# Performance work log

Hardware: AMD Instinct MI355X
Metric: run time of the kernel (lower is better)

Reference implementation:

```python
import jax, jax.numpy as jnp
import numpy as np

B, L, D = 2, 2048, 1024
K, M = 32, 4
H = D // K
AH = 4            # anchor heads
DH = K - AH       # decay heads
CK = 4            # conv kernel size
TOTAL = 2 * D + K + K * M


def setup_inputs() -> dict:
    key = jax.random.key(0)
    ks = jax.random.split(key, 7)
    x = jax.random.normal(ks[0], (B, L, D), jnp.float32)
    mask = jnp.ones((B, L), jnp.float32)
    W_in = jax.random.normal(ks[1], (D, TOTAL), jnp.float32) * 0.02
    conv_w = jax.random.normal(ks[2], (CK, TOTAL), jnp.float32) * 0.1  # depthwise taps
    conv_b = jnp.zeros((TOTAL,), jnp.float32)
    grid = np.linspace(-np.pi / 3, np.pi / 3, M).astype(np.float32)
    theta_base = jnp.asarray(np.tile(grid.reshape(1, 1, 1, 1, M), (1, 1, K, 1, 1)))
    theta_resid_scale = jnp.full((K,), 0.1, jnp.float32)
    dr = np.geomspace(0.001, 0.1, DH).astype(np.float32)
    decay_slopes = jnp.asarray(np.log(np.exp(dr) - 1.0).astype(np.float32))
    ar = np.geomspace(0.01, 0.1, AH).astype(np.float32)
    anchor_slopes = jnp.asarray(np.log(np.exp(ar) - 1.0).astype(np.float32))
    score_scale = jnp.ones((K,), jnp.float32)
    norm_scale = jnp.ones((2 * H * M,), jnp.float32)
    gl = float((2.0 / (H * M + H)) ** 0.5)  # glorot std
    W_re = jax.random.normal(ks[3], (H * M, H), jnp.float32) * gl
    W_im = jax.random.normal(ks[4], (H * M, H), jnp.float32) * gl
    W_out = jax.random.normal(ks[5], (D, D), jnp.float32) * 0.02
    return dict(x=x, mask=mask, W_in=W_in, conv_w=conv_w, conv_b=conv_b,
                theta_base=theta_base, theta_resid_scale=theta_resid_scale,
                decay_slopes=decay_slopes, anchor_slopes=anchor_slopes,
                score_scale=score_scale, norm_scale=norm_scale,
                W_re=W_re, W_im=W_im, W_out=W_out)


def _forward(x, mask, W_in, conv_w, conv_b, theta_base, theta_resid_scale,
             decay_slopes, anchor_slopes, score_scale, norm_scale, W_re, W_im, W_out):
    b, l, d = x.shape
    z = x @ W_in  # (b,l,TOTAL)
    # causal depthwise conv, kernel size CK
    zp = jnp.pad(z, ((0, 0), (CK - 1, 0), (0, 0)))
    z = sum(zp[:, t:t + l, :] * conv_w[t] for t in range(CK)) + conv_b

    x_val = z[..., :D].reshape(b, l, K, H)
    x_gate = jax.nn.silu(z[..., D:2 * D])
    s_raw = z[..., 2 * D:2 * D + K].reshape(b, l, K, 1)
    theta_raw = z[..., 2 * D + K:].reshape(b, l, K, M)

    theta_delta = theta_raw / (1.0 + jnp.abs(theta_raw))
    theta_dyn = theta_base + theta_resid_scale.reshape(1, 1, K, 1, 1) * (
        theta_delta.reshape(b, l, K, 1, M) * jnp.float32(np.pi / 3))

    m = mask[:, :, None, None]
    s_raw = s_raw * m
    x_val = x_val * m

    pos = jnp.arange(l, dtype=jnp.float32)
    slopes_d = jax.nn.softplus(decay_slopes).reshape(1, 1, DH, 1)
    dist_d = jnp.maximum(jnp.float32(l - 1) - pos, 0.0)[None, :, None, None]
    w_decay = jnp.exp(-slopes_d * dist_d)
    slopes_a = jax.nn.softplus(anchor_slopes).reshape(1, 1, AH, 1)
    w_anchor = jnp.exp(-slopes_a * pos[None, :, None, None])
    time_weight = jnp.concatenate([w_decay, w_anchor], axis=2)  # (1,l,K,1)

    p = jnp.exp(jnp.clip(score_scale[None, None, :, None] * s_raw, -20.0, 20.0))
    p = p * m

    phi = x_val[..., None] * theta_dyn  # (b,l,K,H,M)
    cos_b = jnp.cos(phi)
    sin_b = jnp.sin(phi)
    p_w = (p * time_weight)[..., None]  # (b,l,K,1,1)

    flat = (b, l, K * H * M)
    merged = jnp.concatenate([
        (p_w * cos_b).reshape(flat),
        (p_w * sin_b).reshape(flat),
        jnp.broadcast_to(p_w, (b, l, K, H, M)).reshape(flat)], axis=-1)
    cs = jnp.cumsum(merged, axis=1)
    num_re, num_im, den = jnp.split(cs, 3, axis=-1)
    inv_den = 1.0 / jnp.maximum(den, jnp.float32(1e-4))
    re = (num_re * inv_den).reshape(b, l, K, H * M)
    im = (num_im * inv_den).reshape(b, l, K, H * M)

    mean_sq = (jnp.sum(re * re, axis=-1) + jnp.sum(im * im, axis=-1)) * (1.0 / (2.0 * H * M))
    rsq = jax.lax.rsqrt(mean_sq[..., None] + 1e-5)
    y = (re * rsq * norm_scale[:H * M]) @ W_re + (im * rsq * norm_scale[H * M:]) @ W_im  # (b,l,K,H)
    y = y.reshape(b, l, D)
    return (y * x_gate) @ W_out


def reference(x, mask, W_in, conv_w, conv_b, theta_base, theta_resid_scale,
              decay_slopes, anchor_slopes, score_scale, norm_scale, W_re, W_im, W_out):
    return _forward(x, mask, W_in, conv_w, conv_b, theta_base, theta_resid_scale,
                    decay_slopes, anchor_slopes, score_scale, norm_scale, W_re, W_im, W_out)
```

## Files before the change

### kernel.cpp

```cpp
#include <hip/hip_runtime.h>
#include <hip/hip_bf16.h>
#include <math.h>

#define B_ 2
#define L_ 2048
#define D_ 1024
#define K_ 32
#define M_ 4
#define H_ 32
#define AH_ 4
#define DH_ 28
#define CK_ 4
#define TOTAL_ 2208
#define NPAD_ 2304
#define BL_ (B_*L_)
#define CL_ 16
#define NC_ (L_/CL_)
#define CTS_ 280

typedef __attribute__((ext_vector_type(8))) short bf16x8;
typedef __attribute__((ext_vector_type(4))) float f32x4;

static __device__ inline unsigned short f2bu(float f) {
    union { __hip_bfloat16 h; unsigned short u; } cv;
    cv.h = __float2bfloat16(f);
    return cv.u;
}
static __device__ inline float b2f(unsigned short u) {
    union { unsigned short u; __hip_bfloat16 h; } cv;
    cv.u = u;
    return __bfloat162float(cv.h);
}
static __device__ inline float conv4(float bias, const float w[4], float r0, float r1,
                                     float r2, float zc) {
    return fmaf(w[3], zc, fmaf(w[2], r2, fmaf(w[1], r1, fmaf(w[0], r0, bias))));
}

__global__ __launch_bounds__(256) void prep_all(const float* __restrict__ x,
                                                const float* __restrict__ W_in,
                                                const float* __restrict__ Wout,
                                                const float* __restrict__ Wre,
                                                const float* __restrict__ Wim,
                                                const float* __restrict__ nscale,
                                                ushort* __restrict__ x_bf,
                                                ushort* __restrict__ Wt_in,
                                                ushort* __restrict__ Wt_o,
                                                ushort* __restrict__ W2B) {
    __shared__ float tile[64][65];
    int bid = blockIdx.x, t = threadIdx.x;
    if (bid < 4096) {
        int i = bid * 256 + t;
        float4 v = ((const float4*)x)[i];
        ushort4 o;
        o.x = f2bu(v.x); o.y = f2bu(v.y); o.z = f2bu(v.z); o.w = f2bu(v.w);
        *(ushort4*)(x_bf + (size_t)i * 4) = o;
        return;
    }
    const float* src; ushort* dst; int Kd, N, n0, k0;
    if (bid < 4096 + 576) {
        int bb = bid - 4096;
        src = W_in; dst = Wt_in; Kd = 1024; N = TOTAL_;
        n0 = (bb % 36) * 64; k0 = (bb / 36) * 64;
    } else if (bid < 4096 + 576 + 256) {
        int bb = bid - 4096 - 576;
        src = Wout; dst = Wt_o; Kd = 1024; N = 1024;
        n0 = (bb % 16) * 64; k0 = (bb / 16) * 64;
    } else {
        int ch = t;
        float ns = nscale[ch];
        for (int ho = 0; ho < 32; ++ho) {
            float w = (ch < 128) ? Wre[ch * 32 + ho] : Wim[(ch - 128) * 32 + ho];
            W2B[ho * 256 + ch] = f2bu(ns * w);
        }
        return;
    }
#pragma unroll
    for (int i = 0; i < 16; ++i) {
        int idx = t + i * 256;
        int r = idx >> 6, c = idx & 63;
        int gn = n0 + c;
        tile[r][c] = (gn < N) ? src[(size_t)(k0 + r) * N + gn] : 0.f;
    }
    __syncthreads();
#pragma unroll
    for (int i = 0; i < 16; ++i) {
        int idx = t + i * 256;
        int r = idx >> 6, c = idx & 63;
        dst[(size_t)(n0 + r) * Kd + k0 + c] = f2bu(tile[c][r]);
    }
}

template <bool OUT_BF16>
__global__ __launch_bounds__(256) void gemm_bt64(const ushort* __restrict__ A,
                                                 const ushort* __restrict__ Bt,
                                                 void* __restrict__ Cv,
                                                 int Kd, int ldc) {
    __shared__ __align__(16) ushort SB[192 * 32];
    int tid = threadIdx.x;
    int wave = tid >> 6, lane = tid & 63;
    int quad = lane >> 4, l16 = lane & 15;
    int n0 = blockIdx.x * 128, m0 = blockIdx.y * 64;
    int wm = (wave & 1) * 32, wn = (wave >> 1) * 64;
    f32x4 acc[2][4];
#pragma unroll
    for (int i = 0; i < 2; ++i)
#pragma unroll
        for (int j = 0; j < 4; ++j) acc[i][j] = (f32x4){0.f, 0.f, 0.f, 0.f};

    int swzq = quad ^ (l16 & 3);

    for (int k0 = 0; k0 < Kd; k0 += 32) {
#pragma unroll
        for (int i = 0; i < 3; ++i) {
            int s = i * 256 + tid;
            int row = s >> 2;
            int qg = (s & 3) ^ (row & 3);
            const ushort* g = (row < 64) ? A + (size_t)(m0 + row) * Kd + k0 + qg * 8
                                         : Bt + (size_t)(n0 + row - 64) * Kd + k0 + qg * 8;
            __builtin_amdgcn_global_load_lds((const __attribute__((address_space(1))) void*)g,
                                             (__attribute__((address_space(3))) void*)(SB + (size_t)s * 8),
                                             16, 0, 0);
        }
        __syncthreads();
        bf16x8 af[2], bfr[4];
#pragma unroll
        for (int mi = 0; mi < 2; ++mi)
            af[mi] = *(const bf16x8*)(SB + (size_t)(wm + mi * 16 + l16) * 32 + swzq * 8);
#pragma unroll
        for (int ni = 0; ni < 4; ++ni)
            bfr[ni] = *(const bf16x8*)(SB + (size_t)(64 + wn + ni * 16 + l16) * 32 + swzq * 8);
#pragma unroll
        for (int mi = 0; mi < 2; ++mi)
#pragma unroll
            for (int ni = 0; ni < 4; ++ni)
                acc[mi][ni] = __builtin_amdgcn_mfma_f32_16x16x32_bf16(af[mi], bfr[ni], acc[mi][ni], 0, 0, 0);
        __syncthreads();
    }
#pragma unroll
    for (int mi = 0; mi < 2; ++mi)
#pragma unroll
        for (int ni = 0; ni < 4; ++ni)
#pragma unroll
            for (int r = 0; r < 4; ++r) {
                int gm = m0 + wm + mi * 16 + quad * 4 + r;
                int gn = n0 + wn + ni * 16 + l16;
                if (OUT_BF16)
                    ((ushort*)Cv)[(size_t)gm * ldc + gn] = f2bu(acc[mi][ni][r]);
                else
                    ((float*)Cv)[(size_t)gm * ldc + gn] = acc[mi][ni][r];
            }
}

__global__ __launch_bounds__(128) void pass1f(const ushort* __restrict__ z,
                                              const float* __restrict__ mask,
                                              const float* __restrict__ theta_base,
                                              const float* __restrict__ trs_,
                                              const float* __restrict__ dslopes,
                                              const float* __restrict__ aslopes,
                                              const float* __restrict__ sscale_,
                                              const float* __restrict__ conv_w,
                                              const float* __restrict__ conv_b,
                                              const ushort* __restrict__ W2B,
                                              float* __restrict__ cs_re,
                                              float* __restrict__ cs_im,
                                              float* __restrict__ cs_den,
                                              float* __restrict__ vc,
                                              float* __restrict__ ucs) {
    __shared__ __align__(16) ushort ct[CL_ * CTS_];
    int nc = blockIdx.x, k = blockIdx.y, b = blockIdx.z;
    int hm = threadIdx.x;
    int h = hm >> 2, m = hm & 3;
    int bk = b * K_ + k;
    size_t bkL = (size_t)bk * L_;
    int cxv = k * H_ + h, csc = 2 * D_ + k, cth = 2 * D_ + K_ + k * M_ + m;
    float wx[4], ws4[4], wt4[4];
#pragma unroll
    for (int t = 0; t < 4; ++t) {
        wx[t] = conv_w[t * TOTAL_ + cxv];
        ws4[t] = conv_w[t * TOTAL_ + csc];
        wt4[t] = conv_w[t * TOTAL_ + cth];
    }
    float bx = conv_b[cxv], bs = conv_b[csc], bt = conv_b[cth];
    int l0 = nc * CL_;
    float rx[3], rs[3], rt[3];
#pragma unroll
    for (int j = 0; j < 3; ++j) {
        int ls = l0 - 3 + j;
        if (ls >= 0) {
            size_t zo = (size_t)(b * L_ + ls) * NPAD_;
            rx[j] = b2f(z[zo + cxv]); rs[j] = b2f(z[zo + csc]); rt[j] = b2f(z[zo + cth]);
        } else { rx[j] = 0.f; rs[j] = 0.f; rt[j] = 0.f; }
    }
    float raw = (k < DH_) ? dslopes[k] : aslopes[k - DH_];
    float slope = log1pf(__expf(raw));
    float sscale = sscale_[k], trsv = trs_[k], tb = theta_base[k * M_ + m];
    const float PI3 = 1.04719755119659775f;
    float tw = (k < DH_) ? __expf(-slope * (float)(L_ - 1 - l0)) : __expf(-slope * (float)l0);
    float e_s = (k < DH_) ? __expf(slope) : __expf(-slope);
    float are = 0.f, aim = 0.f, aden = 0.f;
#pragma unroll 4
    for (int i = 0; i < CL_; ++i) {
        int l = l0 + i;
        int row = b * L_ + l;
        size_t zo = (size_t)row * NPAD_;
        float zx = b2f(z[zo + cxv]), zs = b2f(z[zo + csc]), zt = b2f(z[zo + cth]);
        float mval = mask[row];
        float xv = conv4(bx, wx, rx[0], rx[1], rx[2], zx) * mval;
        float s_raw = conv4(bs, ws4, rs[0], rs[1], rs[2], zs) * mval;
        float tr = conv4(bt, wt4, rt[0], rt[1], rt[2], zt);
        rx[0] = rx[1]; rx[1] = rx[2]; rx[2] = zx;
        rs[0] = rs[1]; rs[1] = rs[2]; rs[2] = zs;
        rt[0] = rt[1]; rt[1] = rt[2]; rt[2] = zt;
        float arg = fminf(fmaxf(sscale * s_raw, -20.f), 20.f);
        float p = __expf(arg) * mval;
        float pw = p * tw;
        tw *= e_s;
        float td = tr / (1.f + fabsf(tr));
        float theta = tb + trsv * (td * PI3);
        float phi = xv * theta;
        float sv = __sinf(phi), cv = __cosf(phi);
        unsigned short cu_re = f2bu(pw * cv);
        unsigned short cu_im = f2bu(pw * sv);
        are += b2f(cu_re); aim += b2f(cu_im); aden += pw;
        ct[i * CTS_ + hm] = cu_re;
        ct[i * CTS_ + 128 + hm] = cu_im;
    }
    size_t o = ((size_t)(bk * NC_ + nc)) * 128 + hm;
    cs_re[o] = are;
    cs_im[o] = aim;
    if (hm == 0) cs_den[bk * NC_ + nc] = aden;
    __syncthreads();
    int wave = hm >> 6, lane = hm & 63;
    int quad = lane >> 4, l16 = lane & 15;
    f32x4 acc = (f32x4){0.f, 0.f, 0.f, 0.f};
#pragma unroll
    for (int ks = 0; ks < 8; ++ks) {
        bf16x8 af = *(const bf16x8*)(ct + (size_t)l16 * CTS_ + ks * 32 + quad * 8);
        bf16x8 bfr = *(const bf16x8*)(W2B + (size_t)(wave * 16 + l16) * 256 + ks * 32 + quad * 8);
        acc = __builtin_amdgcn_mfma_f32_16x16x32_bf16(af, bfr, acc, 0, 0, 0);
    }
    size_t vbase = (bkL + l0) * 32;
#pragma unroll
    for (int r = 0; r < 4; ++r) {
        int rowv = quad * 4 + r;
        vc[vbase + (size_t)rowv * 32 + wave * 16 + l16] = acc[r];
    }
    float part = acc[0] + acc[1] + acc[2] + acc[3];
    part += __shfl_xor(part, 16, 64);
    part += __shfl_xor(part, 32, 64);
    if (quad == 0) ucs[((size_t)(bk * NC_ + nc)) * 32 + wave * 16 + l16] = part;
}

__global__ void scan2(float* cs_re, float* cs_im, float* cs_den,
                      const float* __restrict__ ucs, float* __restrict__ u_prev) {
    int bid = blockIdx.x, tid = threadIdx.x;
    if (bid < 65) {
        int seq = bid * 256 + tid;
        if (seq >= B_ * K_ * 257) return;
        int bk = seq / 257;
        int ch = seq % 257;
        float* base;
        int stride;
        if (ch < 128) { base = cs_re + (size_t)bk * NC_ * 128 + ch; stride = 128; }
        else if (ch < 256) { base = cs_im + (size_t)bk * NC_ * 128 + (ch - 128); stride = 128; }
        else { base = cs_den + (size_t)bk * NC_; stride = 1; }
        float run = 0.f;
#pragma unroll 4
        for (int i = 0; i < NC_; ++i) {
            float v = base[(size_t)i * stride];
            base[(size_t)i * stride] = run;
            run += v;
        }
    } else {
        int idx = (bid - 65) * 256 + tid;
        int hout = idx & 31;
        int bk = idx >> 5;
        float run = 0.f;
#pragma unroll 8
        for (int nc = 0; nc < NC_; ++nc) {
            size_t o = ((size_t)bk * NC_ + nc) * 32 + hout;
            float v = ucs[o];
            u_prev[o] = run;
            run += v;
        }
    }
}

__global__ __launch_bounds__(64) void scan_k7(const ushort* __restrict__ z,
                                              const float* __restrict__ mask,
                                              const float* __restrict__ theta_base,
                                              const float* __restrict__ trs_,
                                              const float* __restrict__ dslopes,
                                              const float* __restrict__ aslopes,
                                              const float* __restrict__ sscale_,
                                              const float* __restrict__ conv_w,
                                              const float* __restrict__ conv_b,
                                              const float* __restrict__ cs_re,
                                              const float* __restrict__ cs_im,
                                              const float* __restrict__ cs_den,
                                              const float* __restrict__ u_prev,
                                              const float* __restrict__ vc,
                                              ushort* __restrict__ gq) {
    int nc = blockIdx.x, k = blockIdx.y, b = blockIdx.z;
    int lane = threadIdx.x;
    int bk = b * K_ + k;
    size_t bkL = (size_t)bk * L_;
    int h0 = lane >> 2, m = lane & 3;
    int hout = lane & 31;
    int c0 = k * H_ + h0, c1 = k * H_ + 16 + h0;
    int csc = 2 * D_ + k, cth = 2 * D_ + K_ + k * M_ + m, cg = D_ + k * H_ + hout;
    float w0[4], w1[4], ws4[4], wt4[4], wg[4];
#pragma unroll
    for (int t = 0; t < 4; ++t) {
        w0[t] = conv_w[t * TOTAL_ + c0];
        w1[t] = conv_w[t * TOTAL_ + c1];
        ws4[t] = conv_w[t * TOTAL_ + csc];
        wt4[t] = conv_w[t * TOTAL_ + cth];
        wg[t] = conv_w[t * TOTAL_ + cg];
    }
    float b0c = conv_b[c0], b1c = conv_b[c1], bsc = conv_b[csc], btc = conv_b[cth], bgc = conv_b[cg];
    int l0 = nc * CL_;
    float r0[3], r1[3], rs[3], rt[3], rg[3];
#pragma unroll
    for (int j = 0; j < 3; ++j) {
        int ls = l0 - 3 + j;
        if (ls >= 0) {
            size_t zo = (size_t)(b * L_ + ls) * NPAD_;
            r0[j] = b2f(z[zo + c0]); r1[j] = b2f(z[zo + c1]); rs[j] = b2f(z[zo + csc]);
            rt[j] = b2f(z[zo + cth]); rg[j] = b2f(z[zo + cg]);
        } else { r0[j] = 0.f; r1[j] = 0.f; rs[j] = 0.f; rt[j] = 0.f; rg[j] = 0.f; }
    }
    float raw = (k < DH_) ? dslopes[k] : aslopes[k - DH_];
    float slope = log1pf(__expf(raw));
    float sscale = sscale_[k], trsv = trs_[k], tb = theta_base[k * M_ + m];
    const float PI3 = 1.04719755119659775f;
    float tw = (k < DH_) ? __expf(-slope * (float)(L_ - 1 - l0)) : __expf(-slope * (float)l0);
    float e_s = (k < DH_) ? __expf(slope) : __expf(-slope);

    size_t o = ((size_t)(bk * NC_ + nc)) * 128;
    float are0 = cs_re[o + lane];
    float are1 = cs_re[o + 64 + lane];
    float aim0 = cs_im[o + lane];
    float aim1 = cs_im[o + 64 + lane];
    float den = cs_den[bk * NC_ + nc];
    float u = u_prev[((size_t)(bk * NC_ + nc)) * 32 + hout];

#pragma unroll 4
    for (int i = 0; i < CL_; ++i) {
        int l = l0 + i;
        int row = b * L_ + l;
        size_t zo = (size_t)row * NPAD_;
        float z0 = b2f(z[zo + c0]), z1 = b2f(z[zo + c1]), zs = b2f(z[zo + csc]);
        float zt = b2f(z[zo + cth]), zg = b2f(z[zo + cg]);
        float mval = mask[row];
        float xv0 = conv4(b0c, w0, r0[0], r0[1], r0[2], z0) * mval;
        float xv1 = conv4(b1c, w1, r1[0], r1[1], r1[2], z1) * mval;
        float s_raw = conv4(bsc, ws4, rs[0], rs[1], rs[2], zs) * mval;
        float tr = conv4(btc, wt4, rt[0], rt[1], rt[2], zt);
        float gpre = conv4(bgc, wg, rg[0], rg[1], rg[2], zg);
        r0[0] = r0[1]; r0[1] = r0[2]; r0[2] = z0;
        r1[0] = r1[1]; r1[1] = r1[2]; r1[2] = z1;
        rs[0] = rs[1]; rs[1] = rs[2]; rs[2] = zs;
        rt[0] = rt[1]; rt[1] = rt[2]; rt[2] = zt;
        rg[0] = rg[1]; rg[1] = rg[2]; rg[2] = zg;
        float arg = fminf(fmaxf(sscale * s_raw, -20.f), 20.f);
        float p = __expf(arg) * mval;
        float pw = p * tw;
        tw *= e_s;
        float td = tr / (1.f + fabsf(tr));
        float theta = tb + trsv * (td * PI3);
        float s0 = __sinf(xv0 * theta), cv0 = __cosf(xv0 * theta);
        float s1 = __sinf(xv1 * theta), cv1 = __cosf(xv1 * theta);
        float cre0 = b2f(f2bu(pw * cv0)), cim0 = b2f(f2bu(pw * s0));
        float cre1 = b2f(f2bu(pw * cv1)), cim1 = b2f(f2bu(pw * s1));
        are0 += cre0; aim0 += cim0; are1 += cre1; aim1 += cim1;
        den += pw;
        float s = are0 * are0 + are1 * are1 + aim0 * aim0 + aim1 * aim1;
#pragma unroll
        for (int off = 32; off; off >>= 1) s += __shfl_xor(s, off, 64);
        float inv = 1.f / fmaxf(den, 1e-4f);
        float rsq = rsqrtf(inv * inv * s * (1.0f / 256.0f) + 1e-5f);
        float scv = inv * rsq;
        u += vc[(bkL + l) * 32 + hout];
        float y = scv * u;
        float gate = gpre / (1.f + __expf(-gpre));
        if (lane < 32) gq[(size_t)row * D_ + k * H_ + hout] = f2bu(y * gate);
    }
}

extern "C" void kernel_launch(void* const* d_in, const int* in_sizes, int n_in,
                              void* d_out, int out_size, void* d_ws, size_t ws_size,
                              hipStream_t stream) {
    const float* x = (const float*)d_in[0];
    const float* mask = (const float*)d_in[1];
    const float* W_in = (const float*)d_in[2];
    const float* conv_w = (const float*)d_in[3];
    const float* conv_b = (const float*)d_in[4];
    const float* theta_base = (const float*)d_in[5];
    const float* trs = (const float*)d_in[6];
    const float* dsl = (const float*)d_in[7];
    const float* asl = (const float*)d_in[8];
    const float* ssc = (const float*)d_in[9];
    const float* nsc = (const float*)d_in[10];
    const float* Wre = (const float*)d_in[11];
    const float* Wim = (const float*)d_in[12];
    const float* Wout = (const float*)d_in[13];
    float* out = (float*)d_out;

    char* ws = (char*)d_ws;
    ushort* z     = (ushort*)(ws);
    ushort* x_bf  = (ushort*)(ws + 18874368ULL);
    ushort* Wt_in = (ushort*)(ws + 27262976ULL);
    ushort* Wt_o  = (ushort*)(ws + 31981568ULL);
    ushort* W2B   = (ushort*)(ws + 34078720ULL);
    float* vc     = (float*)(ws + 34095104ULL);
    float* cs_re  = (float*)(ws + 50872320ULL);
    float* cs_im  = (float*)(ws + 55066624ULL);
    float* cs_den = (float*)(ws + 59260928ULL);
    float* ucs    = (float*)(ws + 59293696ULL);
    float* u_prev = (float*)(ws + 60342272ULL);
    ushort* gq    = (ushort*)(ws + 61390848ULL);

    prep_all<<<4096 + 576 + 256 + 1, 256, 0, stream>>>(x, W_in, Wout, Wre, Wim, nsc,
                                                       x_bf, Wt_in, Wt_o, W2B);
    gemm_bt64<true><<<dim3(NPAD_ / 128, BL_ / 64), 256, 0, stream>>>(x_bf, Wt_in, z, 1024, NPAD_);
    pass1f<<<dim3(NC_, K_, B_), 128, 0, stream>>>(z, mask, theta_base, trs, dsl, asl, ssc,
                                                  conv_w, conv_b, W2B,
                                                  cs_re, cs_im, cs_den, vc, ucs);
    scan2<<<73, 256, 0, stream>>>(cs_re, cs_im, cs_den, ucs, u_prev);
    scan_k7<<<dim3(NC_, K_, B_), 64, 0, stream>>>(z, mask, theta_base, trs, dsl, asl, ssc,
                                                  conv_w, conv_b, cs_re, cs_im, cs_den,
                                                  u_prev, vc, gq);
    gemm_bt64<false><<<dim3(1024 / 128, BL_ / 64), 256, 0, stream>>>(gq, Wt_o, out, 1024, 1024);
}
```

Before: 256.9 us.

## Precompute conv, theta, and weights once per chunk in shared memory

```diff
diff --git a/kernel.cpp b/kernel.cpp
--- a/kernel.cpp
+++ b/kernel.cpp
@@ -31,9 +31,17 @@
     cv.u = u;
     return __bfloat162float(cv.h);
 }
-static __device__ inline float conv4(float bias, const float w[4], float r0, float r1,
-                                     float r2, float zc) {
-    return fmaf(w[3], zc, fmaf(w[2], r2, fmaf(w[1], r1, fmaf(w[0], r0, bias))));
+
+static __device__ inline float convd(const ushort* z, int blbase, int l, int ch,
+                                     const float* w4, float bias) {
+    float acc = bias;
+#pragma unroll
+    for (int tap = 0; tap < 4; ++tap) {
+        int ls = l - 3 + tap;
+        float zv = (ls >= 0) ? b2f(z[(size_t)(blbase + ls) * NPAD_ + ch]) : 0.f;
+        acc = fmaf(w4[tap], zv, acc);
+    }
+    return acc;
 }
 
 __global__ __launch_bounds__(256) void prep_all(const float* __restrict__ x,
@@ -167,68 +175,85 @@
                                               float* __restrict__ vc,
                                               float* __restrict__ ucs) {
     __shared__ __align__(16) ushort ct[CL_ * CTS_];
+    __shared__ float theta_s[CL_ * 4];
+    __shared__ float pw_s[CL_];
+    __shared__ float xv_s[CL_][33];
+
     int nc = blockIdx.x, k = blockIdx.y, b = blockIdx.z;
     int hm = threadIdx.x;
-    int h = hm >> 2, m = hm & 3;
     int bk = b * K_ + k;
     size_t bkL = (size_t)bk * L_;
-    int cxv = k * H_ + h, csc = 2 * D_ + k, cth = 2 * D_ + K_ + k * M_ + m;
-    float wx[4], ws4[4], wt4[4];
-#pragma unroll
-    for (int t = 0; t < 4; ++t) {
-        wx[t] = conv_w[t * TOTAL_ + cxv];
-        ws4[t] = conv_w[t * TOTAL_ + csc];
-        wt4[t] = conv_w[t * TOTAL_ + cth];
-    }
-    float bx = conv_b[cxv], bs = conv_b[csc], bt = conv_b[cth];
     int l0 = nc * CL_;
-    float rx[3], rs[3], rt[3];
-#pragma unroll
-    for (int j = 0; j < 3; ++j) {
-        int ls = l0 - 3 + j;
-        if (ls >= 0) {
-            size_t zo = (size_t)(b * L_ + ls) * NPAD_;
-            rx[j] = b2f(z[zo + cxv]); rs[j] = b2f(z[zo + csc]); rt[j] = b2f(z[zo + cth]);
-        } else { rx[j] = 0.f; rs[j] = 0.f; rt[j] = 0.f; }
-    }
+    int blb = b * L_;
+    const float PI3 = 1.04719755119659775f;
+
     float raw = (k < DH_) ? dslopes[k] : aslopes[k - DH_];
     float slope = log1pf(__expf(raw));
-    float sscale = sscale_[k], trsv = trs_[k], tb = theta_base[k * M_ + m];
-    const float PI3 = 1.04719755119659775f;
-    float tw = (k < DH_) ? __expf(-slope * (float)(L_ - 1 - l0)) : __expf(-slope * (float)l0);
-    float e_s = (k < DH_) ? __expf(slope) : __expf(-slope);
-    float are = 0.f, aim = 0.f, aden = 0.f;
-#pragma unroll 4
+
+    if (hm < 64) {
+        int li = hm >> 2, m = hm & 3;
+        int l = l0 + li;
+        int cth = 2 * D_ + K_ + k * M_ + m;
+        float wt[4];
+#pragma unroll
+        for (int t = 0; t < 4; ++t) wt[t] = conv_w[t * TOTAL_ + cth];
+        float tr = convd(z, blb, l, cth, wt, conv_b[cth]);
+        float td = tr / (1.f + fabsf(tr));
+        theta_s[li * 4 + m] = theta_base[k * M_ + m] + trs_[k] * (td * PI3);
+    }
+    if (hm >= 64 && hm < 64 + CL_) {
+        int li = hm - 64;
+        int l = l0 + li;
+        int csc = 2 * D_ + k;
+        float wsv[4];
+#pragma unroll
+        for (int t = 0; t < 4; ++t) wsv[t] = conv_w[t * TOTAL_ + csc];
+        float mval = mask[blb + l];
+        float s_raw = convd(z, blb, l, csc, wsv, conv_b[csc]) * mval;
+        float arg = fminf(fmaxf(sscale_[k] * s_raw, -20.f), 20.f);
+        float p = __expf(arg) * mval;
+        float tw = (k < DH_) ? __expf(-slope * (float)(L_ - 1 - l)) : __expf(-slope * (float)l);
+        pw_s[li] = p * tw;
+    }
+    {
+        int h = hm & 31, lset = hm >> 5;
+        int cxv = k * H_ + h;
+        float wxv[4];
+#pragma unroll
+        for (int t = 0; t < 4; ++t) wxv[t] = conv_w[t * TOTAL_ + cxv];
+        float bxv = conv_b[cxv];
+#pragma unroll
+        for (int j = 0; j < 4; ++j) {
+            int li = lset * 4 + j;
+            int l = l0 + li;
+            float xv = convd(z, blb, l, cxv, wxv, bxv) * mask[blb + l];
+            xv_s[li][h] = xv;
+        }
+    }
+    __syncthreads();
+
+    int h = hm >> 2, m = hm & 3;
+    float are = 0.f, aim = 0.f;
+#pragma unroll
     for (int i = 0; i < CL_; ++i) {
-        int l = l0 + i;
-        int row = b * L_ + l;
-        size_t zo = (size_t)row * NPAD_;
-        float zx = b2f(z[zo + cxv]), zs = b2f(z[zo + csc]), zt = b2f(z[zo + cth]);
-        float mval = mask[row];
-        float xv = conv4(bx, wx, rx[0], rx[1], rx[2], zx) * mval;
-        float s_raw = conv4(bs, ws4, rs[0], rs[1], rs[2], zs) * mval;
-        float tr = conv4(bt, wt4, rt[0], rt[1], rt[2], zt);
-        rx[0] = rx[1]; rx[1] = rx[2]; rx[2] = zx;
-        rs[0] = rs[1]; rs[1] = rs[2]; rs[2] = zs;
-        rt[0] = rt[1]; rt[1] = rt[2]; rt[2] = zt;
-        float arg = fminf(fmaxf(sscale * s_raw, -20.f), 20.f);
-        float p = __expf(arg) * mval;
-        float pw = p * tw;
-        tw *= e_s;
-        float td = tr / (1.f + fabsf(tr));
-        float theta = tb + trsv * (td * PI3);
-        float phi = xv * theta;
+        float phi = xv_s[i][h] * theta_s[i * 4 + m];
+        float pw = pw_s[i];
         float sv = __sinf(phi), cv = __cosf(phi);
         unsigned short cu_re = f2bu(pw * cv);
         unsigned short cu_im = f2bu(pw * sv);
-        are += b2f(cu_re); aim += b2f(cu_im); aden += pw;
+        are += b2f(cu_re); aim += b2f(cu_im);
         ct[i * CTS_ + hm] = cu_re;
         ct[i * CTS_ + 128 + hm] = cu_im;
     }
     size_t o = ((size_t)(bk * NC_ + nc)) * 128 + hm;
     cs_re[o] = are;
     cs_im[o] = aim;
-    if (hm == 0) cs_den[bk * NC_ + nc] = aden;
+    if (hm == 0) {
+        float aden = 0.f;
+#pragma unroll
+        for (int i = 0; i < CL_; ++i) aden += pw_s[i];
+        cs_den[bk * NC_ + nc] = aden;
+    }
     __syncthreads();
     int wave = hm >> 6, lane = hm & 63;
     int quad = lane >> 4, l16 = lane & 15;
@@ -301,41 +326,71 @@
                                               const float* __restrict__ u_prev,
                                               const float* __restrict__ vc,
                                               ushort* __restrict__ gq) {
+    __shared__ float theta_s[CL_ * 4];
+    __shared__ float pw_s[CL_];
+    __shared__ float xv_s[CL_][33];
+    __shared__ float gate_s[CL_][33];
+
     int nc = blockIdx.x, k = blockIdx.y, b = blockIdx.z;
     int lane = threadIdx.x;
     int bk = b * K_ + k;
     size_t bkL = (size_t)bk * L_;
-    int h0 = lane >> 2, m = lane & 3;
-    int hout = lane & 31;
-    int c0 = k * H_ + h0, c1 = k * H_ + 16 + h0;
-    int csc = 2 * D_ + k, cth = 2 * D_ + K_ + k * M_ + m, cg = D_ + k * H_ + hout;
-    float w0[4], w1[4], ws4[4], wt4[4], wg[4];
-#pragma unroll
-    for (int t = 0; t < 4; ++t) {
-        w0[t] = conv_w[t * TOTAL_ + c0];
-        w1[t] = conv_w[t * TOTAL_ + c1];
-        ws4[t] = conv_w[t * TOTAL_ + csc];
-        wt4[t] = conv_w[t * TOTAL_ + cth];
-        wg[t] = conv_w[t * TOTAL_ + cg];
-    }
-    float b0c = conv_b[c0], b1c = conv_b[c1], bsc = conv_b[csc], btc = conv_b[cth], bgc = conv_b[cg];
     int l0 = nc * CL_;
-    float r0[3], r1[3], rs[3], rt[3], rg[3];
-#pragma unroll
-    for (int j = 0; j < 3; ++j) {
-        int ls = l0 - 3 + j;
-        if (ls >= 0) {
-            size_t zo = (size_t)(b * L_ + ls) * NPAD_;
-            r0[j] = b2f(z[zo + c0]); r1[j] = b2f(z[zo + c1]); rs[j] = b2f(z[zo + csc]);
-            rt[j] = b2f(z[zo + cth]); rg[j] = b2f(z[zo + cg]);
-        } else { r0[j] = 0.f; r1[j] = 0.f; rs[j] = 0.f; rt[j] = 0.f; rg[j] = 0.f; }
-    }
+    int blb = b * L_;
+    const float PI3 = 1.04719755119659775f;
+
     float raw = (k < DH_) ? dslopes[k] : aslopes[k - DH_];
     float slope = log1pf(__expf(raw));
-    float sscale = sscale_[k], trsv = trs_[k], tb = theta_base[k * M_ + m];
-    const float PI3 = 1.04719755119659775f;
-    float tw = (k < DH_) ? __expf(-slope * (float)(L_ - 1 - l0)) : __expf(-slope * (float)l0);
-    float e_s = (k < DH_) ? __expf(slope) : __expf(-slope);
+
+    {
+        int li = lane >> 2, m = lane & 3;
+        int l = l0 + li;
+        int cth = 2 * D_ + K_ + k * M_ + m;
+        float wt[4];
+#pragma unroll
+        for (int t = 0; t < 4; ++t) wt[t] = conv_w[t * TOTAL_ + cth];
+        float tr = convd(z, blb, l, cth, wt, conv_b[cth]);
+        float td = tr / (1.f + fabsf(tr));
+        theta_s[li * 4 + m] = theta_base[k * M_ + m] + trs_[k] * (td * PI3);
+    }
+    if (lane < CL_) {
+        int l = l0 + lane;
+        int csc = 2 * D_ + k;
+        float wsv[4];
+#pragma unroll
+        for (int t = 0; t < 4; ++t) wsv[t] = conv_w[t * TOTAL_ + csc];
+        float mval = mask[blb + l];
+        float s_raw = convd(z, blb, l, csc, wsv, conv_b[csc]) * mval;
+        float arg = fminf(fmaxf(sscale_[k] * s_raw, -20.f), 20.f);
+        float p = __expf(arg) * mval;
+        float tw = (k < DH_) ? __expf(-slope * (float)(L_ - 1 - l)) : __expf(-slope * (float)l);
+        pw_s[lane] = p * tw;
+    }
+    {
+        int h = lane & 31, lset = lane >> 5;
+        int cxv = k * H_ + h;
+        int cg = D_ + k * H_ + h;
+        float wxv[4], wg[4];
+#pragma unroll
+        for (int t = 0; t < 4; ++t) {
+            wxv[t] = conv_w[t * TOTAL_ + cxv];
+            wg[t] = conv_w[t * TOTAL_ + cg];
+        }
+        float bxv = conv_b[cxv], bg = conv_b[cg];
+#pragma unroll
+        for (int j = 0; j < 8; ++j) {
+            int li = lset * 8 + j;
+            int l = l0 + li;
+            float xv = convd(z, blb, l, cxv, wxv, bxv) * mask[blb + l];
+            xv_s[li][h] = xv;
+            float gp = convd(z, blb, l, cg, wg, bg);
+            gate_s[li][h] = gp / (1.f + __expf(-gp));
+        }
+    }
+    __syncthreads();
+
+    int h0 = lane >> 2, h1 = 16 + (lane >> 2), m = lane & 3;
+    int hout = lane & 31;
 
     size_t o = ((size_t)(bk * NC_ + nc)) * 128;
     float are0 = cs_re[o + lane];
@@ -348,29 +403,12 @@
 #pragma unroll 4
     for (int i = 0; i < CL_; ++i) {
         int l = l0 + i;
-        int row = b * L_ + l;
-        size_t zo = (size_t)row * NPAD_;
-        float z0 = b2f(z[zo + c0]), z1 = b2f(z[zo + c1]), zs = b2f(z[zo + csc]);
-        float zt = b2f(z[zo + cth]), zg = b2f(z[zo + cg]);
-        float mval = mask[row];
-        float xv0 = conv4(b0c, w0, r0[0], r0[1], r0[2], z0) * mval;
-        float xv1 = conv4(b1c, w1, r1[0], r1[1], r1[2], z1) * mval;
-        float s_raw = conv4(bsc, ws4, rs[0], rs[1], rs[2], zs) * mval;
-        float tr = conv4(btc, wt4, rt[0], rt[1], rt[2], zt);
-        float gpre = conv4(bgc, wg, rg[0], rg[1], rg[2], zg);
-        r0[0] = r0[1]; r0[1] = r0[2]; r0[2] = z0;
-        r1[0] = r1[1]; r1[1] = r1[2]; r1[2] = z1;
-        rs[0] = rs[1]; rs[1] = rs[2]; rs[2] = zs;
-        rt[0] = rt[1]; rt[1] = rt[2]; rt[2] = zt;
-        rg[0] = rg[1]; rg[1] = rg[2]; rg[2] = zg;
-        float arg = fminf(fmaxf(sscale * s_raw, -20.f), 20.f);
-        float p = __expf(arg) * mval;
-        float pw = p * tw;
-        tw *= e_s;
-        float td = tr / (1.f + fabsf(tr));
-        float theta = tb + trsv * (td * PI3);
-        float s0 = __sinf(xv0 * theta), cv0 = __cosf(xv0 * theta);
-        float s1 = __sinf(xv1 * theta), cv1 = __cosf(xv1 * theta);
+        float th = theta_s[i * 4 + m];
+        float pw = pw_s[i];
+        float phi0 = xv_s[i][h0] * th;
+        float phi1 = xv_s[i][h1] * th;
+        float s0 = __sinf(phi0), cv0 = __cosf(phi0);
+        float s1 = __sinf(phi1), cv1 = __cosf(phi1);
         float cre0 = b2f(f2bu(pw * cv0)), cim0 = b2f(f2bu(pw * s0));
         float cre1 = b2f(f2bu(pw * cv1)), cim1 = b2f(f2bu(pw * s1));
         are0 += cre0; aim0 += cim0; are1 += cre1; aim1 += cim1;
@@ -380,11 +418,9 @@
         for (int off = 32; off; off >>= 1) s += __shfl_xor(s, off, 64);
         float inv = 1.f / fmaxf(den, 1e-4f);
         float rsq = rsqrtf(inv * inv * s * (1.0f / 256.0f) + 1e-5f);
-        float scv = inv * rsq;
         u += vc[(bkL + l) * 32 + hout];
-        float y = scv * u;
-        float gate = gpre / (1.f + __expf(-gpre));
-        if (lane < 32) gq[(size_t)row * D_ + k * H_ + hout] = f2bu(y * gate);
+        float gv = inv * rsq * u * gate_s[i][hout];
+        if (lane < 32) gq[(size_t)(blb + l) * D_ + k * H_ + hout] = f2bu(gv);
     }
 }
 
```

After: 259.7 us. About the same (+1.1%).
